# Optimization experiments

Measured on AMD Instinct MI355X. Metric: run time of the kernel, lower is better.

Reference implementation:

```python
import jax, jax.numpy as jnp
import numpy as np

B, S, D, H = 2, 2048, 1024, 16
DK = D // H  # 64
SQRT_DK = DK ** 0.5
NEG = -1e9


def setup_inputs() -> dict:
    key = jax.random.key(0)
    ks = jax.random.split(key, 7)
    scale = 1.0 / np.sqrt(D)
    return {
        "x": jax.random.normal(ks[0], (B, S, D), jnp.float32),
        "encoder_output": jax.random.normal(ks[1], (B, S, D), jnp.float32),
        "mask": jax.random.randint(ks[2], (B, S), 0, 2, jnp.int32),
        "WQ": jax.random.normal(ks[3], (D, D), jnp.float32) * scale,
        "WK": jax.random.normal(ks[4], (D, D), jnp.float32) * scale,
        "WV": jax.random.normal(ks[5], (D, D), jnp.float32) * scale,
        "WO": jax.random.normal(ks[6], (D, D), jnp.float32) * scale,
    }


def reference(x, encoder_output, mask, WQ, WK, WV, WO):
    b, s, d = x.shape
    # project and split heads: (b, h, s, dk)
    q = (x @ WQ).reshape(b, s, H, DK).transpose(0, 2, 1, 3)
    k = (encoder_output @ WK).reshape(b, s, H, DK).transpose(0, 2, 1, 3)
    v = (encoder_output @ WV).reshape(b, s, H, DK).transpose(0, 2, 1, 3)
    # scores: (b, h, s_q, s_k)
    scores = jnp.einsum('bhqd,bhkd->bhqk', q, k) / SQRT_DK
    # future mask (strict upper triangle) + padding mask broadcast over key dim
    future = jnp.triu(jnp.ones((s, s), jnp.int32), 1)  # (s, s)
    m = mask[:, None, :, None] + future[None, None, :, :]  # (b, 1->h, s_q, s_k)
    scores = jnp.where(m != 0, NEG, scores)
    attn = jax.nn.softmax(scores, axis=-1)
    # context: (b, s, h, dk) -> (b, s, d)
    ctx = jnp.einsum('bhqk,bhkd->bqhd', attn, v).reshape(b, s, d)
    return ctx @ WO
```

## Files before the change

### kernel.cpp

```cpp
#include <hip/hip_runtime.h>
#include <hip/hip_bf16.h>

constexpr int B = 2, S = 2048, D = 1024, H = 16, DK = 64;
constexpr int M = B * S;
constexpr float LOG2E = 1.44269504088896f;
constexpr float NEGBIG = -3.0e38f;
constexpr float QSCALE = 0.125f * LOG2E;

using short8 = __attribute__((ext_vector_type(8))) short;
using short4v = __attribute__((ext_vector_type(4))) short;
using f32x4 = __attribute__((ext_vector_type(4))) float;

#define GLOBAL_AS __attribute__((address_space(1)))
#define LDS_AS __attribute__((address_space(3)))

__device__ __forceinline__ void gll16(const void* g, void* l) {
  __builtin_amdgcn_global_load_lds((const GLOBAL_AS void*)g, (LDS_AS void*)l, 16, 0, 0);
}

__device__ __forceinline__ short f2bf(float f) {
  __hip_bfloat16 h = __float2bfloat16(f);
  short s;
  __builtin_memcpy(&s, &h, 2);
  return s;
}
__device__ __forceinline__ unsigned pack2bf(float a, float b) {
  return (unsigned)(unsigned short)f2bf(a) | ((unsigned)(unsigned short)f2bf(b) << 16);
}

__global__ __launch_bounds__(256) void prep_kernel(const float* __restrict__ x,
                                                   const float* __restrict__ enc,
                                                   const float* __restrict__ W0,
                                                   const float* __restrict__ W1,
                                                   const float* __restrict__ W2,
                                                   const float* __restrict__ W3,
                                                   short* __restrict__ xb,
                                                   short* __restrict__ encb,
                                                   short* __restrict__ Wt) {
  __shared__ float t[64][65];
  const int bx = blockIdx.x;
  if (bx < 8192) {
    const float4* src = (const float4*)((bx & 4096) ? enc : x);
    short4v* dst = (short4v*)((bx & 4096) ? encb : xb);
    const int i = (bx & 4095) * 256 + threadIdx.x;
    const float4 v = src[i];
    short4v o;
    o[0] = f2bf(v.x); o[1] = f2bf(v.y); o[2] = f2bf(v.z); o[3] = f2bf(v.w);
    dst[i] = o;
  } else {
    const int idx = bx - 8192;
    const int z = idx >> 8, rem = idx & 255;
    const float* W = z == 0 ? W0 : z == 1 ? W1 : z == 2 ? W2 : W3;
    short* dstw = Wt + (size_t)z * D * D;
    const int n0 = (rem & 15) * 64, k0 = (rem >> 4) * 64;
    const int lx = threadIdx.x & 63, ly = threadIdx.x >> 6;
    #pragma unroll
    for (int r = 0; r < 64; r += 4)
      t[r + ly][lx] = W[(size_t)(k0 + r + ly) * D + n0 + lx];
    __syncthreads();
    #pragma unroll
    for (int r = 0; r < 64; r += 4)
      dstw[(size_t)(n0 + r + ly) * D + k0 + lx] = f2bf(t[lx][r + ly]);
  }
}

__global__ __launch_bounds__(256) void gemm_qkv_kernel(const short* __restrict__ A0,
                                                       const short* __restrict__ A1,
                                                       const short* __restrict__ Wts,
                                                       short* __restrict__ Cv,
                                                       float* __restrict__ vsum) {
  __shared__ short As[2][4][128][8];
  __shared__ short Bs[2][4][128][8];
  const int z = blockIdx.z;
  const short* __restrict__ A = z ? A1 : A0;
  const short* __restrict__ Bt = Wts + (size_t)z * D * D;
  const float oscale = (z == 0) ? QSCALE : 1.0f;

  const int tid = threadIdx.x;
  const int lane = tid & 63, wid = tid >> 6;
  const int l15 = lane & 15, lg = lane >> 4;
  const int row0 = blockIdx.x * 128, col0 = blockIdx.y * 128;
  const int wm = wid >> 1, wn = wid & 1;
  f32x4 acc[4][4] = {};

  auto stage = [&](int k0, int nb) {
    #pragma unroll
    for (int it = 0; it < 2; ++it) {
      const int c = tid + it * 256;
      const int row = c & 127, kc2 = c >> 7;
      gll16(&A[(size_t)(row0 + row) * D + k0 + kc2 * 8],
            (char*)As + nb * 8192 + (wid * 64 + it * 256) * 16);
      gll16(&Bt[(size_t)(col0 + row) * D + k0 + kc2 * 8],
            (char*)Bs + nb * 8192 + (wid * 64 + it * 256) * 16);
    }
  };

  stage(0, 0);
  __syncthreads();
  int cur = 0;
  for (int t = 0; t < D / 32; ++t) {
    if (t < D / 32 - 1) stage((t + 1) * 32, cur ^ 1);
    short8 af[4], bfr[4];
    #pragma unroll
    for (int m = 0; m < 4; ++m) af[m] = *(const short8*)&As[cur][lg][wm * 64 + m * 16 + l15][0];
    #pragma unroll
    for (int n = 0; n < 4; ++n) bfr[n] = *(const short8*)&Bs[cur][lg][wn * 64 + n * 16 + l15][0];
    #pragma unroll
    for (int m = 0; m < 4; ++m)
      #pragma unroll
      for (int n = 0; n < 4; ++n)
        acc[m][n] = __builtin_amdgcn_mfma_f32_16x16x32_bf16(af[m], bfr[n], acc[m][n], 0, 0, 0);
    __syncthreads();
    cur ^= 1;
  }
  #pragma unroll
  for (int m = 0; m < 4; ++m) {
    #pragma unroll
    for (int r = 0; r < 4; ++r) {
      const int row = row0 + wm * 64 + m * 16 + 4 * lg + r;
      #pragma unroll
      for (int n = 0; n < 4; ++n) {
        const int col = col0 + wn * 64 + n * 16 + l15;
        Cv[(size_t)z * M * D + (size_t)row * D + col] = f2bf(acc[m][n][r] * oscale);
      }
    }
  }
  if (z == 2) {
    const int bidx = row0 >> 11;
    #pragma unroll
    for (int n = 0; n < 4; ++n) {
      float s = 0.f;
      #pragma unroll
      for (int m = 0; m < 4; ++m)
        s += acc[m][n][0] + acc[m][n][1] + acc[m][n][2] + acc[m][n][3];
      s += __shfl_xor(s, 16);
      s += __shfl_xor(s, 32);
      if (lg == 0) atomicAdd(&vsum[(size_t)bidx * D + col0 + wn * 64 + n * 16 + l15], s);
    }
  }
}

__global__ __launch_bounds__(256) void gemmO_kernel(const short* __restrict__ A,
                                                    const short* __restrict__ Bt,
                                                    float* __restrict__ C) {
  __shared__ short As[2][4][128][8];
  __shared__ short Bs[2][4][64][8];
  const int tid = threadIdx.x;
  const int lane = tid & 63, wid = tid >> 6;
  const int l15 = lane & 15, lg = lane >> 4;
  const int row0 = blockIdx.x * 128, col0 = blockIdx.y * 64;
  const int wm = wid >> 1, wn = wid & 1;
  f32x4 acc[4][2] = {};

  auto stage = [&](int k0, int nb) {
    #pragma unroll
    for (int it = 0; it < 2; ++it) {
      const int c = tid + it * 256;
      const int row = c & 127, kc2 = c >> 7;
      gll16(&A[(size_t)(row0 + row) * D + k0 + kc2 * 8],
            (char*)As + nb * 8192 + (wid * 64 + it * 256) * 16);
    }
    gll16(&Bt[(size_t)(col0 + lane) * D + k0 + wid * 8],
          (char*)Bs + nb * 4096 + wid * 1024);
  };

  stage(0, 0);
  __syncthreads();
  int cur = 0;
  for (int t = 0; t < D / 32; ++t) {
    if (t < D / 32 - 1) stage((t + 1) * 32, cur ^ 1);
    short8 af[4], bfr[2];
    #pragma unroll
    for (int m = 0; m < 4; ++m) af[m] = *(const short8*)&As[cur][lg][wm * 64 + m * 16 + l15][0];
    #pragma unroll
    for (int n = 0; n < 2; ++n) bfr[n] = *(const short8*)&Bs[cur][lg][wn * 32 + n * 16 + l15][0];
    #pragma unroll
    for (int m = 0; m < 4; ++m)
      #pragma unroll
      for (int n = 0; n < 2; ++n)
        acc[m][n] = __builtin_amdgcn_mfma_f32_16x16x32_bf16(af[m], bfr[n], acc[m][n], 0, 0, 0);
    __syncthreads();
    cur ^= 1;
  }
  #pragma unroll
  for (int m = 0; m < 4; ++m)
    #pragma unroll
    for (int r = 0; r < 4; ++r) {
      const int row = row0 + wm * 64 + m * 16 + 4 * lg + r;
      #pragma unroll
      for (int n = 0; n < 2; ++n)
        C[(size_t)row * D + col0 + wn * 32 + n * 16 + l15] = acc[m][n][r];
    }
}

__device__ __forceinline__ int keyof(int c, int i) {
  return ((c >> 1) << 5) + ((i >> 2) << 3) + ((c & 1) << 2) + (i & 3);
}
__device__ __forceinline__ int vt_byte(int kc, int d, int ksb) {
  return kc * 1024 + ((d ^ (kc & 7)) << 4) + ksb * 2;
}

__global__ __launch_bounds__(512, 4) void attn_kernel(const short* __restrict__ Qb,
                                                      const short* __restrict__ Kb,
                                                      const short* __restrict__ Vb,
                                                      const int* __restrict__ maskp,
                                                      const float* __restrict__ vsum,
                                                      short* __restrict__ ctxb) {
  __shared__ char KsBuf[2][16384];
  __shared__ char VtBuf[2][16384];
  const int h = blockIdx.x, iblk = blockIdx.y, b = blockIdx.z;
  const int qtA = iblk, qtB = 31 - iblk;
  const int tid = threadIdx.x, lane = tid & 63, wid = tid >> 6;
  const int grp = wid >> 2, wq = wid & 3;
  const int qt = grp ? qtB : qtA;
  const int l15 = lane & 15, lg = lane >> 4;

  short8 qf[2];
  {
    const size_t o = (size_t)(b * S + qt * 64 + wq * 16 + l15) * D + h * DK;
    qf[0] = *(const short8*)&Qb[o + lg * 8];
    qf[1] = *(const short8*)&Qb[o + 32 + lg * 8];
  }
  float m = NEGBIG, l = 0.f;
  f32x4 cx[4] = {};

  const int kkey = keyof(lg, l15);
  const int vu = tid & 63, dv = tid >> 6;
  const int vh = vu >> 5, vl = vu & 31;
  const int vkc = vl >> 2, vksb = (vl & 3) * 2;

  auto stageK = [&](int jc, int nb) {
    const size_t base = (size_t)(b * S + jc * 128 + kkey) * D + h * DK + wid * 8;
    gll16(&Kb[base], (char*)KsBuf + nb * 16384 + wid * 1024);
    gll16(&Kb[base + (size_t)64 * D], (char*)KsBuf + nb * 16384 + 8192 + wid * 1024);
  };
  auto loadV = [&](int jc, short8& va, short8& vb2) {
    const size_t vb0 = (size_t)(b * S + jc * 128 + 2 * vu) * D + h * DK + dv * 8;
    va = *(const short8*)&Vb[vb0];
    vb2 = *(const short8*)&Vb[vb0 + D];
  };
  auto writeV = [&](int nb, const short8& va, const short8& vb2) {
    char* dst = (char*)VtBuf + nb * 16384 + vh * 8192;
    #pragma unroll
    for (int i = 0; i < 8; ++i) {
      const unsigned w = (unsigned)(unsigned short)va[i] | ((unsigned)(unsigned short)vb2[i] << 16);
      *(unsigned*)(dst + vt_byte(vkc, dv * 8 + i, vksb)) = w;
    }
  };

  auto tile_pair = [&](int nb, bool do1, bool diag0, bool diag1) {
    const char* ks0 = (const char*)KsBuf + nb * 16384;
    const char* ks1 = ks0 + 8192;
    const char* vt0 = (const char*)VtBuf + nb * 16384;
    const char* vt1 = vt0 + 8192;
    f32x4 sa0[4], sa1[4];
    #pragma unroll
    for (int c = 0; c < 4; ++c) {
      const short8 kf0 = *(const short8*)(ks0 + lg * 1024 + c * 256 + l15 * 16);
      const short8 kf1 = *(const short8*)(ks0 + (4 + lg) * 1024 + c * 256 + l15 * 16);
      f32x4 zz = {0.f, 0.f, 0.f, 0.f};
      zz = __builtin_amdgcn_mfma_f32_16x16x32_bf16(kf0, qf[0], zz, 0, 0, 0);
      zz = __builtin_amdgcn_mfma_f32_16x16x32_bf16(kf1, qf[1], zz, 0, 0, 0);
      sa0[c] = zz;
    }
    if (do1) {
      #pragma unroll
      for (int c = 0; c < 4; ++c) {
        const short8 kf0 = *(const short8*)(ks1 + lg * 1024 + c * 256 + l15 * 16);
        const short8 kf1 = *(const short8*)(ks1 + (4 + lg) * 1024 + c * 256 + l15 * 16);
        f32x4 zz = {0.f, 0.f, 0.f, 0.f};
        zz = __builtin_amdgcn_mfma_f32_16x16x32_bf16(kf0, qf[0], zz, 0, 0, 0);
        zz = __builtin_amdgcn_mfma_f32_16x16x32_bf16(kf1, qf[1], zz, 0, 0, 0);
        sa1[c] = zz;
      }
    }
    const int ql = wq * 16 + l15;
    if (diag0) {
      #pragma unroll
      for (int c = 0; c < 4; ++c)
        #pragma unroll
        for (int r = 0; r < 4; ++r)
          if (((c >> 1) << 5) + (lg << 3) + ((c & 1) << 2) + r > ql) sa0[c][r] = NEGBIG;
    }
    if (do1 && diag1) {
      #pragma unroll
      for (int c = 0; c < 4; ++c)
        #pragma unroll
        for (int r = 0; r < 4; ++r)
          if (((c >> 1) << 5) + (lg << 3) + ((c & 1) << 2) + r > ql) sa1[c][r] = NEGBIG;
    }
    float pm = sa0[0][0];
    #pragma unroll
    for (int c = 0; c < 4; ++c)
      #pragma unroll
      for (int r = 0; r < 4; ++r) pm = fmaxf(pm, sa0[c][r]);
    if (do1)
      #pragma unroll
      for (int c = 0; c < 4; ++c)
        #pragma unroll
        for (int r = 0; r < 4; ++r) pm = fmaxf(pm, sa1[c][r]);
    pm = fmaxf(pm, __shfl_xor(pm, 16));
    pm = fmaxf(pm, __shfl_xor(pm, 32));
    if (pm > m + 8.f) {
      const float sc = exp2f(m - pm);
      l *= sc;
      #pragma unroll
      for (int dt = 0; dt < 4; ++dt) cx[dt] *= sc;
      m = pm;
    }
    float rs = 0.f;
    #pragma unroll
    for (int c = 0; c < 4; ++c)
      #pragma unroll
      for (int r = 0; r < 4; ++r) {
        const float p = exp2f(sa0[c][r] - m);
        sa0[c][r] = p;
        rs += p;
      }
    if (do1)
      #pragma unroll
      for (int c = 0; c < 4; ++c)
        #pragma unroll
        for (int r = 0; r < 4; ++r) {
          const float p = exp2f(sa1[c][r] - m);
          sa1[c][r] = p;
          rs += p;
        }
    rs += __shfl_xor(rs, 16);
    rs += __shfl_xor(rs, 32);
    l += rs;
    {
      short8 pf[2];
      #pragma unroll
      for (int kk = 0; kk < 2; ++kk)
        #pragma unroll
        for (int jj = 0; jj < 8; ++jj)
          pf[kk][jj] = f2bf(sa0[kk * 2 + (jj >> 2)][jj & 3]);
      #pragma unroll
      for (int kk = 0; kk < 2; ++kk)
        #pragma unroll
        for (int dt = 0; dt < 4; ++dt) {
          const short8 vf = *(const short8*)(vt0 + vt_byte(kk * 4 + lg, dt * 16 + l15, 0));
          cx[dt] = __builtin_amdgcn_mfma_f32_16x16x32_bf16(vf, pf[kk], cx[dt], 0, 0, 0);
        }
    }
    if (do1) {
      short8 pf[2];
      #pragma unroll
      for (int kk = 0; kk < 2; ++kk)
        #pragma unroll
        for (int jj = 0; jj < 8; ++jj)
          pf[kk][jj] = f2bf(sa1[kk * 2 + (jj >> 2)][jj & 3]);
      #pragma unroll
      for (int kk = 0; kk < 2; ++kk)
        #pragma unroll
        for (int dt = 0; dt < 4; ++dt) {
          const short8 vf = *(const short8*)(vt1 + vt_byte(kk * 4 + lg, dt * 16 + l15, 0));
          cx[dt] = __builtin_amdgcn_mfma_f32_16x16x32_bf16(vf, pf[kk], cx[dt], 0, 0, 0);
        }
    }
  };

  const int nB = (qtB >> 1) + 1;
  {
    short8 va, vb2;
    stageK(0, 0);
    loadV(0, va, vb2);
    writeV(0, va, vb2);
  }
  __syncthreads();
  int cur = 0;
  for (int jc = 0; jc < nB; ++jc) {
    short8 nva, nvb;
    if (jc + 1 < nB) { stageK(jc + 1, cur ^ 1); loadV(jc + 1, nva, nvb); }
    const int t0 = 2 * jc, t1 = 2 * jc + 1;
    if (t0 <= qt) tile_pair(cur, t1 <= qt, t0 == qt, t1 == qt);
    if (jc + 1 < nB) writeV(cur ^ 1, nva, nvb);
    __syncthreads();
    cur ^= 1;
  }

  {
    const int qg = qt * 64 + wq * 16 + l15;
    const int mq = maskp[b * S + qg];
    const float inv = 1.0f / l;
    constexpr float vscale = 1.0f / S;
    short* orow = &ctxb[(size_t)(b * S + qg) * D + h * DK];
    const float* vmb = &vsum[(size_t)b * D + h * DK];
    #pragma unroll
    for (int dt = 0; dt < 4; ++dt)
      #pragma unroll
      for (int p2 = 0; p2 < 2; ++p2) {
        const int d = dt * 16 + 4 * lg + p2 * 2;
        const float v0 = mq ? vmb[d] * vscale     : cx[dt][p2 * 2] * inv;
        const float v1 = mq ? vmb[d + 1] * vscale : cx[dt][p2 * 2 + 1] * inv;
        *(unsigned*)&orow[d] = pack2bf(v0, v1);
      }
  }
}

extern "C" void kernel_launch(void* const* d_in, const int* in_sizes, int n_in,
                              void* d_out, int out_size, void* d_ws, size_t ws_size,
                              hipStream_t stream) {
  (void)in_sizes; (void)n_in; (void)out_size; (void)ws_size;
  const float* x   = (const float*)d_in[0];
  const float* enc = (const float*)d_in[1];
  const int*   msk = (const int*)d_in[2];
  const float* WQ  = (const float*)d_in[3];
  const float* WK  = (const float*)d_in[4];
  const float* WV  = (const float*)d_in[5];
  const float* WO  = (const float*)d_in[6];
  float* out = (float*)d_out;

  char* ws = (char*)d_ws;
  const size_t MB = 1u << 20;
  short* xb    = (short*)(ws + 0);
  short* encb  = (short*)(ws + 8 * MB);
  short* Qb    = (short*)(ws + 16 * MB);
  short* WQt   = (short*)(ws + 40 * MB);
  float* vsum  = (float*)(ws + 48 * MB);
  short* Kb    = Qb + (size_t)M * D;
  short* Vb    = Kb + (size_t)M * D;
  short* WOt   = WQt + (size_t)3 * D * D;
  short* ctxb  = xb;

  hipMemsetAsync(vsum, 0, (size_t)B * D * sizeof(float), stream);

  prep_kernel<<<dim3(9216), 256, 0, stream>>>(x, enc, WQ, WK, WV, WO, xb, encb, WQt);

  gemm_qkv_kernel<<<dim3(M / 128, D / 128, 3), 256, 0, stream>>>(xb, encb, WQt, Qb, vsum);

  attn_kernel<<<dim3(H, 16, B), 512, 0, stream>>>(Qb, Kb, Vb, msk, vsum, ctxb);

  gemmO_kernel<<<dim3(M / 128, D / 64), 256, 0, stream>>>(ctxb, WOt, out);
}
```

Baseline: 167.5 us.

## Triple-buffer GEMM K-loops and remap attention to 128-row query tiles

Both GEMM kernels move from double to triple LDS buffering with prefetch distance two. They replace __syncthreads with explicit s_waitcnt vmcnt plus s_barrier so global-to-LDS loads stay in flight across one iteration. The attention kernel drops the paired query-tile (iblk, 31-iblk) balancing and gives each block one 128-row query tile, with all 8 waves sharing each 128-key K/V chunk. Blocks are launched largest-first on a 1D grid. This changes the diagonal masking and the load balance, and the hand-written vmcnt counts must match the number of issued loads exactly.

```diff
diff --git a/kernel.cpp b/kernel.cpp
--- a/kernel.cpp
+++ b/kernel.cpp
@@ -69,8 +69,8 @@
                                                        const short* __restrict__ Wts,
                                                        short* __restrict__ Cv,
                                                        float* __restrict__ vsum) {
-  __shared__ short As[2][4][128][8];
-  __shared__ short Bs[2][4][128][8];
+  __shared__ short As[3][4][128][8];
+  __shared__ short Bs[3][4][128][8];
   const int z = blockIdx.z;
   const short* __restrict__ A = z ? A1 : A0;
   const short* __restrict__ Bt = Wts + (size_t)z * D * D;
@@ -82,6 +82,7 @@
   const int row0 = blockIdx.x * 128, col0 = blockIdx.y * 128;
   const int wm = wid >> 1, wn = wid & 1;
   f32x4 acc[4][4] = {};
+  constexpr int NSTEP = D / 32;
 
   auto stage = [&](int k0, int nb) {
     #pragma unroll
@@ -96,10 +97,12 @@
   };
 
   stage(0, 0);
-  __syncthreads();
-  int cur = 0;
-  for (int t = 0; t < D / 32; ++t) {
-    if (t < D / 32 - 1) stage((t + 1) * 32, cur ^ 1);
+  stage(32, 1);
+  for (int t = 0; t < NSTEP; ++t) {
+    if (t < NSTEP - 1) asm volatile("s_waitcnt vmcnt(4)\ns_barrier" ::: "memory");
+    else               asm volatile("s_waitcnt vmcnt(0)\ns_barrier" ::: "memory");
+    if (t + 2 < NSTEP) stage((t + 2) * 32, (t + 2) % 3);
+    const int cur = t % 3;
     short8 af[4], bfr[4];
     #pragma unroll
     for (int m = 0; m < 4; ++m) af[m] = *(const short8*)&As[cur][lg][wm * 64 + m * 16 + l15][0];
@@ -110,8 +113,6 @@
       #pragma unroll
       for (int n = 0; n < 4; ++n)
         acc[m][n] = __builtin_amdgcn_mfma_f32_16x16x32_bf16(af[m], bfr[n], acc[m][n], 0, 0, 0);
-    __syncthreads();
-    cur ^= 1;
   }
   #pragma unroll
   for (int m = 0; m < 4; ++m) {
@@ -143,14 +144,15 @@
 __global__ __launch_bounds__(256) void gemmO_kernel(const short* __restrict__ A,
                                                     const short* __restrict__ Bt,
                                                     float* __restrict__ C) {
-  __shared__ short As[2][4][128][8];
-  __shared__ short Bs[2][4][64][8];
+  __shared__ short As[3][4][128][8];
+  __shared__ short Bs[3][4][64][8];
   const int tid = threadIdx.x;
   const int lane = tid & 63, wid = tid >> 6;
   const int l15 = lane & 15, lg = lane >> 4;
   const int row0 = blockIdx.x * 128, col0 = blockIdx.y * 64;
   const int wm = wid >> 1, wn = wid & 1;
   f32x4 acc[4][2] = {};
+  constexpr int NSTEP = D / 32;
 
   auto stage = [&](int k0, int nb) {
     #pragma unroll
@@ -165,10 +167,12 @@
   };
 
   stage(0, 0);
-  __syncthreads();
-  int cur = 0;
-  for (int t = 0; t < D / 32; ++t) {
-    if (t < D / 32 - 1) stage((t + 1) * 32, cur ^ 1);
+  stage(32, 1);
+  for (int t = 0; t < NSTEP; ++t) {
+    if (t < NSTEP - 1) asm volatile("s_waitcnt vmcnt(3)\ns_barrier" ::: "memory");
+    else               asm volatile("s_waitcnt vmcnt(0)\ns_barrier" ::: "memory");
+    if (t + 2 < NSTEP) stage((t + 2) * 32, (t + 2) % 3);
+    const int cur = t % 3;
     short8 af[4], bfr[2];
     #pragma unroll
     for (int m = 0; m < 4; ++m) af[m] = *(const short8*)&As[cur][lg][wm * 64 + m * 16 + l15][0];
@@ -179,8 +183,6 @@
       #pragma unroll
       for (int n = 0; n < 2; ++n)
         acc[m][n] = __builtin_amdgcn_mfma_f32_16x16x32_bf16(af[m], bfr[n], acc[m][n], 0, 0, 0);
-    __syncthreads();
-    cur ^= 1;
   }
   #pragma unroll
   for (int m = 0; m < 4; ++m)
@@ -208,16 +210,17 @@
                                                       short* __restrict__ ctxb) {
   __shared__ char KsBuf[2][16384];
   __shared__ char VtBuf[2][16384];
-  const int h = blockIdx.x, iblk = blockIdx.y, b = blockIdx.z;
-  const int qtA = iblk, qtB = 31 - iblk;
+  const int bid = blockIdx.x;
+  const int qt = 15 - (bid >> 5);
+  const int bh = bid & 31;
+  const int b = bh >> 4, h = bh & 15;
   const int tid = threadIdx.x, lane = tid & 63, wid = tid >> 6;
-  const int grp = wid >> 2, wq = wid & 3;
-  const int qt = grp ? qtB : qtA;
   const int l15 = lane & 15, lg = lane >> 4;
+  const int ql = wid * 16 + l15;
 
   short8 qf[2];
   {
-    const size_t o = (size_t)(b * S + qt * 64 + wq * 16 + l15) * D + h * DK;
+    const size_t o = (size_t)(b * S + qt * 128 + ql) * D + h * DK;
     qf[0] = *(const short8*)&Qb[o + lg * 8];
     qf[1] = *(const short8*)&Qb[o + 32 + lg * 8];
   }
@@ -248,7 +251,7 @@
     }
   };
 
-  auto tile_pair = [&](int nb, bool do1, bool diag0, bool diag1) {
+  auto tile_pair = [&](int nb, bool do1, bool mask0, bool mask1) {
     const char* ks0 = (const char*)KsBuf + nb * 16384;
     const char* ks1 = ks0 + 8192;
     const char* vt0 = (const char*)VtBuf + nb * 16384;
@@ -274,20 +277,19 @@
         sa1[c] = zz;
       }
     }
-    const int ql = wq * 16 + l15;
-    if (diag0) {
+    if (mask0) {
       #pragma unroll
       for (int c = 0; c < 4; ++c)
         #pragma unroll
         for (int r = 0; r < 4; ++r)
           if (((c >> 1) << 5) + (lg << 3) + ((c & 1) << 2) + r > ql) sa0[c][r] = NEGBIG;
     }
-    if (do1 && diag1) {
+    if (do1 && mask1) {
       #pragma unroll
       for (int c = 0; c < 4; ++c)
         #pragma unroll
         for (int r = 0; r < 4; ++r)
-          if (((c >> 1) << 5) + (lg << 3) + ((c & 1) << 2) + r > ql) sa1[c][r] = NEGBIG;
+          if (64 + ((c >> 1) << 5) + (lg << 3) + ((c & 1) << 2) + r > ql) sa1[c][r] = NEGBIG;
     }
     float pm = sa0[0][0];
     #pragma unroll
@@ -361,7 +363,6 @@
     }
   };
 
-  const int nB = (qtB >> 1) + 1;
   {
     short8 va, vb2;
     stageK(0, 0);
@@ -370,18 +371,18 @@
   }
   __syncthreads();
   int cur = 0;
-  for (int jc = 0; jc < nB; ++jc) {
+  for (int jc = 0; jc <= qt; ++jc) {
     short8 nva, nvb;
-    if (jc + 1 < nB) { stageK(jc + 1, cur ^ 1); loadV(jc + 1, nva, nvb); }
-    const int t0 = 2 * jc, t1 = 2 * jc + 1;
-    if (t0 <= qt) tile_pair(cur, t1 <= qt, t0 == qt, t1 == qt);
-    if (jc + 1 < nB) writeV(cur ^ 1, nva, nvb);
+    if (jc < qt) { stageK(jc + 1, cur ^ 1); loadV(jc + 1, nva, nvb); }
+    const bool diag = (jc == qt), hi = (wid >= 4);
+    tile_pair(cur, !diag || hi, diag && !hi, diag && hi);
+    if (jc < qt) writeV(cur ^ 1, nva, nvb);
     __syncthreads();
     cur ^= 1;
   }
 
   {
-    const int qg = qt * 64 + wq * 16 + l15;
+    const int qg = qt * 128 + ql;
     const int mq = maskp[b * S + qg];
     const float inv = 1.0f / l;
     constexpr float vscale = 1.0f / S;
@@ -430,7 +431,7 @@
 
   gemm_qkv_kernel<<<dim3(M / 128, D / 128, 3), 256, 0, stream>>>(xb, encb, WQt, Qb, vsum);
 
-  attn_kernel<<<dim3(H, 16, B), 512, 0, stream>>>(Qb, Kb, Vb, msk, vsum, ctxb);
+  attn_kernel<<<dim3(512), 512, 0, stream>>>(Qb, Kb, Vb, msk, vsum, ctxb);
 
   gemmO_kernel<<<dim3(M / 128, D / 64), 256, 0, stream>>>(ctxb, WOt, out);
 }
```

New measurement: 166.4 us. No clear change (-0.6%).

## Pre-transpose V globally and read K/V directly from global memory in attention

Applied to the files above, without the earlier changes.

Adds a separate kernel that transposes V into a head-major, sequence-contiguous layout, reusing the encoder bf16 buffer. The attention kernel drops LDS staging and double buffering for K and V. Each wave now loads its MFMA fragments straight from global memory and relies on the cache for reuse across the 8 waves. Work is remapped so each block handles one 128-row query tile, with a heavy-first block ordering instead of paired query tiles. This removes LDS writes and barriers but adds an extra kernel launch and more global and L2 traffic per wave.

```diff
diff --git a/kernel.cpp b/kernel.cpp
--- a/kernel.cpp
+++ b/kernel.cpp
@@ -140,6 +140,34 @@
   }
 }
 
+__global__ __launch_bounds__(256) void vtrans_kernel(const short* __restrict__ Vb,
+                                                     short* __restrict__ vt) {
+  __shared__ short t[64][68];
+  const int s0 = blockIdx.x * 64;
+  const int bh = blockIdx.y;
+  const int b = bh >> 4, h = bh & 15;
+  const int tid = threadIdx.x;
+  #pragma unroll
+  for (int p = 0; p < 4; ++p) {
+    const int idx = tid + p * 256;
+    const int sl = idx >> 4, d4 = idx & 15;
+    const short4v v = *(const short4v*)&Vb[(size_t)(b * S + s0 + sl) * D + h * DK + d4 * 4];
+    *(short4v*)&t[sl][d4 * 4] = v;
+  }
+  __syncthreads();
+  #pragma unroll
+  for (int p = 0; p < 4; ++p) {
+    const int idx = tid + p * 256;
+    const int dk = idx >> 4, s4 = idx & 15;
+    short4v v;
+    v[0] = t[s4 * 4 + 0][dk];
+    v[1] = t[s4 * 4 + 1][dk];
+    v[2] = t[s4 * 4 + 2][dk];
+    v[3] = t[s4 * 4 + 3][dk];
+    *(short4v*)&vt[(size_t)(h * DK + dk) * M + b * S + s0 + s4 * 4] = v;
+  }
+}
+
 __global__ __launch_bounds__(256) void gemmO_kernel(const short* __restrict__ A,
                                                     const short* __restrict__ Bt,
                                                     float* __restrict__ C) {
@@ -196,68 +224,46 @@
 __device__ __forceinline__ int keyof(int c, int i) {
   return ((c >> 1) << 5) + ((i >> 2) << 3) + ((c & 1) << 2) + (i & 3);
 }
-__device__ __forceinline__ int vt_byte(int kc, int d, int ksb) {
-  return kc * 1024 + ((d ^ (kc & 7)) << 4) + ksb * 2;
-}
 
 __global__ __launch_bounds__(512, 4) void attn_kernel(const short* __restrict__ Qb,
                                                       const short* __restrict__ Kb,
-                                                      const short* __restrict__ Vb,
+                                                      const short* __restrict__ vt,
                                                       const int* __restrict__ maskp,
                                                       const float* __restrict__ vsum,
                                                       short* __restrict__ ctxb) {
-  __shared__ char KsBuf[2][16384];
-  __shared__ char VtBuf[2][16384];
-  const int h = blockIdx.x, iblk = blockIdx.y, b = blockIdx.z;
-  const int qtA = iblk, qtB = 31 - iblk;
+  const int bid = blockIdx.x;
+  const int qt = (bid < 256) ? 15 - (bid >> 5) : (bid >> 5) - 8;
+  const int bh = bid & 31;
+  const int b = bh >> 4, h = bh & 15;
   const int tid = threadIdx.x, lane = tid & 63, wid = tid >> 6;
-  const int grp = wid >> 2, wq = wid & 3;
-  const int qt = grp ? qtB : qtA;
   const int l15 = lane & 15, lg = lane >> 4;
+  const int ql = wid * 16 + l15;
+  const bool hi = (wid >= 4);
 
   short8 qf[2];
   {
-    const size_t o = (size_t)(b * S + qt * 64 + wq * 16 + l15) * D + h * DK;
+    const size_t o = (size_t)(b * S + qt * 128 + ql) * D + h * DK;
     qf[0] = *(const short8*)&Qb[o + lg * 8];
     qf[1] = *(const short8*)&Qb[o + 32 + lg * 8];
   }
   float m = NEGBIG, l = 0.f;
   f32x4 cx[4] = {};
 
-  const int kkey = keyof(lg, l15);
-  const int vu = tid & 63, dv = tid >> 6;
-  const int vh = vu >> 5, vl = vu & 31;
-  const int vkc = vl >> 2, vksb = (vl & 3) * 2;
-
-  auto stageK = [&](int jc, int nb) {
-    const size_t base = (size_t)(b * S + jc * 128 + kkey) * D + h * DK + wid * 8;
-    gll16(&Kb[base], (char*)KsBuf + nb * 16384 + wid * 1024);
-    gll16(&Kb[base + (size_t)64 * D], (char*)KsBuf + nb * 16384 + 8192 + wid * 1024);
-  };
-  auto loadV = [&](int jc, short8& va, short8& vb2) {
-    const size_t vb0 = (size_t)(b * S + jc * 128 + 2 * vu) * D + h * DK + dv * 8;
-    va = *(const short8*)&Vb[vb0];
-    vb2 = *(const short8*)&Vb[vb0 + D];
-  };
-  auto writeV = [&](int nb, const short8& va, const short8& vb2) {
-    char* dst = (char*)VtBuf + nb * 16384 + vh * 8192;
-    #pragma unroll
-    for (int i = 0; i < 8; ++i) {
-      const unsigned w = (unsigned)(unsigned short)va[i] | ((unsigned)(unsigned short)vb2[i] << 16);
-      *(unsigned*)(dst + vt_byte(vkc, dv * 8 + i, vksb)) = w;
-    }
-  };
-
-  auto tile_pair = [&](int nb, bool do1, bool diag0, bool diag1) {
-    const char* ks0 = (const char*)KsBuf + nb * 16384;
-    const char* ks1 = ks0 + 8192;
-    const char* vt0 = (const char*)VtBuf + nb * 16384;
-    const char* vt1 = vt0 + 8192;
+  int keyc[4];
+  #pragma unroll
+  for (int c = 0; c < 4; ++c) keyc[c] = keyof(c, l15);
+
+  for (int jc = 0; jc <= qt; ++jc) {
+    const bool diag = (jc == qt);
+    const bool do1 = !diag || hi;
+    const size_t krow0 = (size_t)b * S + jc * 128;
     f32x4 sa0[4], sa1[4];
+
     #pragma unroll
     for (int c = 0; c < 4; ++c) {
-      const short8 kf0 = *(const short8*)(ks0 + lg * 1024 + c * 256 + l15 * 16);
-      const short8 kf1 = *(const short8*)(ks0 + (4 + lg) * 1024 + c * 256 + l15 * 16);
+      const short* kp = &Kb[(krow0 + keyc[c]) * D + h * DK + lg * 8];
+      const short8 kf0 = *(const short8*)kp;
+      const short8 kf1 = *(const short8*)(kp + 32);
       f32x4 zz = {0.f, 0.f, 0.f, 0.f};
       zz = __builtin_amdgcn_mfma_f32_16x16x32_bf16(kf0, qf[0], zz, 0, 0, 0);
       zz = __builtin_amdgcn_mfma_f32_16x16x32_bf16(kf1, qf[1], zz, 0, 0, 0);
@@ -266,29 +272,30 @@
     if (do1) {
       #pragma unroll
       for (int c = 0; c < 4; ++c) {
-        const short8 kf0 = *(const short8*)(ks1 + lg * 1024 + c * 256 + l15 * 16);
-        const short8 kf1 = *(const short8*)(ks1 + (4 + lg) * 1024 + c * 256 + l15 * 16);
+        const short* kp = &Kb[(krow0 + 64 + keyc[c]) * D + h * DK + lg * 8];
+        const short8 kf0 = *(const short8*)kp;
+        const short8 kf1 = *(const short8*)(kp + 32);
         f32x4 zz = {0.f, 0.f, 0.f, 0.f};
         zz = __builtin_amdgcn_mfma_f32_16x16x32_bf16(kf0, qf[0], zz, 0, 0, 0);
         zz = __builtin_amdgcn_mfma_f32_16x16x32_bf16(kf1, qf[1], zz, 0, 0, 0);
         sa1[c] = zz;
       }
     }
-    const int ql = wq * 16 + l15;
-    if (diag0) {
+    if (diag && !hi) {
       #pragma unroll
       for (int c = 0; c < 4; ++c)
         #pragma unroll
         for (int r = 0; r < 4; ++r)
           if (((c >> 1) << 5) + (lg << 3) + ((c & 1) << 2) + r > ql) sa0[c][r] = NEGBIG;
     }
-    if (do1 && diag1) {
+    if (diag && hi) {
       #pragma unroll
       for (int c = 0; c < 4; ++c)
         #pragma unroll
         for (int r = 0; r < 4; ++r)
-          if (((c >> 1) << 5) + (lg << 3) + ((c & 1) << 2) + r > ql) sa1[c][r] = NEGBIG;
-    }
+          if (64 + ((c >> 1) << 5) + (lg << 3) + ((c & 1) << 2) + r > ql) sa1[c][r] = NEGBIG;
+    }
+
     float pm = sa0[0][0];
     #pragma unroll
     for (int c = 0; c < 4; ++c)
@@ -329,6 +336,7 @@
     rs += __shfl_xor(rs, 16);
     rs += __shfl_xor(rs, 32);
     l += rs;
+
     {
       short8 pf[2];
       #pragma unroll
@@ -340,7 +348,8 @@
       for (int kk = 0; kk < 2; ++kk)
         #pragma unroll
         for (int dt = 0; dt < 4; ++dt) {
-          const short8 vf = *(const short8*)(vt0 + vt_byte(kk * 4 + lg, dt * 16 + l15, 0));
+          const short8 vf = *(const short8*)&vt[(size_t)(h * DK + dt * 16 + l15) * M +
+                                                krow0 + kk * 32 + lg * 8];
           cx[dt] = __builtin_amdgcn_mfma_f32_16x16x32_bf16(vf, pf[kk], cx[dt], 0, 0, 0);
         }
     }
@@ -355,33 +364,15 @@
       for (int kk = 0; kk < 2; ++kk)
         #pragma unroll
         for (int dt = 0; dt < 4; ++dt) {
-          const short8 vf = *(const short8*)(vt1 + vt_byte(kk * 4 + lg, dt * 16 + l15, 0));
+          const short8 vf = *(const short8*)&vt[(size_t)(h * DK + dt * 16 + l15) * M +
+                                                krow0 + 64 + kk * 32 + lg * 8];
           cx[dt] = __builtin_amdgcn_mfma_f32_16x16x32_bf16(vf, pf[kk], cx[dt], 0, 0, 0);
         }
     }
-  };
-
-  const int nB = (qtB >> 1) + 1;
+  }
+
   {
-    short8 va, vb2;
-    stageK(0, 0);
-    loadV(0, va, vb2);
-    writeV(0, va, vb2);
-  }
-  __syncthreads();
-  int cur = 0;
-  for (int jc = 0; jc < nB; ++jc) {
-    short8 nva, nvb;
-    if (jc + 1 < nB) { stageK(jc + 1, cur ^ 1); loadV(jc + 1, nva, nvb); }
-    const int t0 = 2 * jc, t1 = 2 * jc + 1;
-    if (t0 <= qt) tile_pair(cur, t1 <= qt, t0 == qt, t1 == qt);
-    if (jc + 1 < nB) writeV(cur ^ 1, nva, nvb);
-    __syncthreads();
-    cur ^= 1;
-  }
-
-  {
-    const int qg = qt * 64 + wq * 16 + l15;
+    const int qg = qt * 128 + ql;
     const int mq = maskp[b * S + qg];
     const float inv = 1.0f / l;
     constexpr float vscale = 1.0f / S;
@@ -423,6 +414,7 @@
   short* Vb    = Kb + (size_t)M * D;
   short* WOt   = WQt + (size_t)3 * D * D;
   short* ctxb  = xb;
+  short* vt    = encb;
 
   hipMemsetAsync(vsum, 0, (size_t)B * D * sizeof(float), stream);
 
@@ -430,7 +422,9 @@
 
   gemm_qkv_kernel<<<dim3(M / 128, D / 128, 3), 256, 0, stream>>>(xb, encb, WQt, Qb, vsum);
 
-  attn_kernel<<<dim3(H, 16, B), 512, 0, stream>>>(Qb, Kb, Vb, msk, vsum, ctxb);
+  vtrans_kernel<<<dim3(S / 64, B * H), 256, 0, stream>>>(Vb, vt);
+
+  attn_kernel<<<dim3(512), 512, 0, stream>>>(Qb, Kb, vt, msk, vsum, ctxb);
 
   gemmO_kernel<<<dim3(M / 128, D / 64), 256, 0, stream>>>(ctxb, WOt, out);
 }
```

Result: slower. 236.2 us (+41.0%).
